# Kernel optimization log

Hardware: AMD Instinct MI355X
Metric: run time of the kernel (lower is better)

Reference implementation:

```python
import jax, jax.numpy as jnp
import numpy as np

N_NODES = 10000
N_EDGES = 70000
IN_DIM = 10
HEADS = 6
LIN_OUT = 254
GAT_DIMS = [(256, 508), (512, 250), (256, 120), (128, 20)]  # (in_dim, out_dim) per DeformGAT
NEG_SLOPE = 0.2


def setup_inputs() -> dict:
    key = jax.random.key(0)
    ks = jax.random.split(key, 8)
    inp = {}
    inp["data"] = jax.random.normal(ks[0], (N_NODES, IN_DIM), dtype=jnp.float32)
    inp["edge_idx"] = jax.random.randint(ks[1], (2, N_EDGES), 0, N_NODES)
    inp["bd_mask"] = jax.random.randint(ks[2], (N_NODES,), 0, 2) > 0
    inp["poly_mesh"] = 0
    inp["W_lin"] = jax.random.normal(ks[3], (IN_DIM, LIN_OUT), dtype=jnp.float32) * 0.05
    inp["b_lin"] = jnp.zeros((LIN_OUT,), dtype=jnp.float32)
    for i, (din, dout) in enumerate(GAT_DIMS):
        k1, k2, k3 = jax.random.split(ks[4 + i], 3)
        inp[f"W{i+1}"] = jax.random.normal(k1, (din, HEADS * dout), dtype=jnp.float32) * 0.05
        inp[f"asrc{i+1}"] = jax.random.normal(k2, (HEADS, dout), dtype=jnp.float32) * 0.05
        inp[f"adst{i+1}"] = jax.random.normal(k3, (HEADS, dout), dtype=jnp.float32) * 0.05
    return inp


def deform_gat(coord, feat, src, dst, bd_mask, W, a_src, a_dst, n):
    """One DeformGAT layer: GAT attention over edge list; features aggregated
    (head-averaged, SELU); coords moved to attention-weighted neighbor centroid,
    boundary nodes pinned."""
    H, C = a_src.shape
    x = (feat @ W).reshape(-1, H, C)                       # [N,H,C]
    a_s = jnp.einsum('nhc,hc->nh', x, a_src)               # [N,H]
    a_d = jnp.einsum('nhc,hc->nh', x, a_dst)               # [N,H]
    e = jax.nn.leaky_relu(a_s[src] + a_d[dst], NEG_SLOPE)  # [E,H]
    # segment softmax over incoming edges of each dst node
    m = jax.ops.segment_max(e, dst, num_segments=n)
    m = jnp.where(jnp.isfinite(m), m, 0.0)
    ex = jnp.exp(e - m[dst])
    denom = jax.ops.segment_sum(ex, dst, num_segments=n)
    alpha = ex / jnp.where(denom[dst] > 0, denom[dst], 1.0)        # [E,H]
    agg = jax.ops.segment_sum(alpha[:, :, None] * x[src], dst, num_segments=n)  # [N,H,C]
    out_feat = jax.nn.selu(agg.mean(axis=1))                       # [N,C]
    am = alpha.mean(axis=1)                                        # [E]
    new_coord = jax.ops.segment_sum(am[:, None] * coord[src], dst, num_segments=n)  # [N,2]
    out_coord = jnp.where(bd_mask[:, None], coord, new_coord)
    return out_coord, out_feat


def reference(data, edge_idx, bd_mask, poly_mesh, W_lin, b_lin,
              W1, asrc1, adst1, W2, asrc2, adst2,
              W3, asrc3, adst3, W4, asrc4, adst4):
    n = data.shape[0]
    coords = data[:, 0:2]
    src, dst = edge_idx[0], edge_idx[1]
    h = jax.nn.selu(data @ W_lin + b_lin)                  # [N,254]
    t1 = jnp.concatenate([coords, h], axis=1)              # [N,256]
    c1, f1 = deform_gat(coords, t1, src, dst, bd_mask, W1, asrc1, adst1, n)
    t2 = jnp.concatenate([c1, coords, f1], axis=1)         # [N,512]
    c2, f2 = deform_gat(c1, t2, src, dst, bd_mask, W2, asrc2, adst2, n)
    t3 = jnp.concatenate([c2, c1, coords, f2], axis=1)     # [N,256]
    c3, f3 = deform_gat(c2, t3, src, dst, bd_mask, W3, asrc3, adst3, n)
    t4 = jnp.concatenate([c3, c2, c1, coords, f3], axis=1) # [N,128]
    c4, f4 = deform_gat(c3, t4, src, dst, bd_mask, W4, asrc4, adst4, n)
    return c4
```

## Files before the change

kernel.cpp:

```cpp
#include <hip/hip_runtime.h>
#include <hip/hip_bf16.h>

#define N_NODES 10000
#define N_EDGES 70000
#define HEADS 6
#define MPAD 10112
#define SELU_SCALE 1.0507009873554805f
#define SELU_ALPHA  1.6732632423543772f
#define NEG_SLOPE 0.2f

typedef __attribute__((ext_vector_type(8))) __bf16 bf16x8;
typedef __attribute__((ext_vector_type(4))) float f32x4;

__device__ __forceinline__ float selu_f(float x) {
    return x > 0.f ? SELU_SCALE * x : SELU_SCALE * SELU_ALPHA * (__expf(x) - 1.f);
}
__device__ __forceinline__ unsigned short f2bf(float f) {
    __hip_bfloat16 h = __float2bfloat16(f);
    return __builtin_bit_cast(unsigned short, h);
}
__device__ __forceinline__ float bf2f(unsigned short u) {
    unsigned int x = ((unsigned int)u) << 16;
    return __builtin_bit_cast(float, x);
}

__global__ void count_edges_k(const int* __restrict__ dstv, int* __restrict__ counts) {
    int e = blockIdx.x * blockDim.x + threadIdx.x;
    if (e < N_EDGES) atomicAdd(&counts[dstv[e]], 1);
}

__global__ __launch_bounds__(1024) void scan_k(const int* __restrict__ counts, int* __restrict__ offs) {
    __shared__ int part[1024];
    int tid = threadIdx.x;
    const int per = (N_NODES + 1023) / 1024;
    int start = tid * per;
    int s = 0;
    for (int i = 0; i < per; ++i) { int idx = start + i; if (idx < N_NODES) s += counts[idx]; }
    part[tid] = s;
    __syncthreads();
    for (int off = 1; off < 1024; off <<= 1) {
        int v = (tid >= off) ? part[tid - off] : 0;
        __syncthreads();
        part[tid] += v;
        __syncthreads();
    }
    int run = part[tid] - s;
    for (int i = 0; i < per; ++i) {
        int idx = start + i;
        if (idx < N_NODES) { offs[idx] = run; run += counts[idx]; }
    }
    if (tid == 0) offs[N_NODES] = part[1023];
}

__global__ void fill_csr_k(const int* __restrict__ srcv, const int* __restrict__ dstv,
                           const int* __restrict__ offs,
                           int* __restrict__ cursor, int* __restrict__ srcs) {
    int e = blockIdx.x * blockDim.x + threadIdx.x;
    if (e < N_EDGES) {
        int d = dstv[e];
        int pos = atomicAdd(&cursor[d], 1);
        srcs[offs[d] + pos] = srcv[e];
    }
}

__global__ __launch_bounds__(256) void prep_proj_k(
    const float* __restrict__ data, const float* __restrict__ W, const float* __restrict__ b,
    float* __restrict__ coords0, unsigned short* __restrict__ t1,
    const float* __restrict__ wsf, const float* __restrict__ wdf,
    float* __restrict__ a_s, float* __restrict__ a_d) {
    const int wid = threadIdx.x >> 6, lane = threadIdx.x & 63;
    const int n = blockIdx.x * 4 + wid;
    if (n >= N_NODES) return;
    const int c0 = lane * 4;
    const float* dr = data + (size_t)n * 10;

    float vals[4];
#pragma unroll
    for (int q = 0; q < 4; ++q) {
        int c = c0 + q;
        if (c < 2) {
            vals[q] = dr[c];
        } else {
            int cc = c - 2;
            float acc = b[cc];
#pragma unroll
            for (int k = 0; k < 10; ++k) acc += dr[k] * W[k * 254 + cc];
            vals[q] = selu_f(acc);
        }
    }
    uint2 pk;
    pk.x = (unsigned int)f2bf(vals[0]) | ((unsigned int)f2bf(vals[1]) << 16);
    pk.y = (unsigned int)f2bf(vals[2]) | ((unsigned int)f2bf(vals[3]) << 16);
    *(uint2*)(t1 + (size_t)n * 256 + c0) = pk;
    if (lane == 0) {
        coords0[2 * n] = vals[0];
        coords0[2 * n + 1] = vals[1];
    }

    float s[HEADS] = {}, d[HEADS] = {};
#pragma unroll
    for (int q = 0; q < 4; ++q) {
        float v = bf2f(f2bf(vals[q]));
        const float* ws = wsf + (size_t)(c0 + q) * HEADS;
        const float* wd = wdf + (size_t)(c0 + q) * HEADS;
#pragma unroll
        for (int h = 0; h < HEADS; ++h) {
            s[h] += v * ws[h];
            d[h] += v * wd[h];
        }
    }
#pragma unroll
    for (int off = 32; off > 0; off >>= 1) {
#pragma unroll
        for (int h = 0; h < HEADS; ++h) {
            s[h] += __shfl_xor(s[h], off);
            d[h] += __shfl_xor(d[h], off);
        }
    }
    if (lane == 0) {
#pragma unroll
        for (int h = 0; h < HEADS; ++h) {
            a_s[n * HEADS + h] = s[h];
            a_d[n * HEADS + h] = d[h];
        }
    }
}

__global__ __launch_bounds__(256) void weights_prep_k(
    const float* __restrict__ W0, const float* __restrict__ s0v, const float* __restrict__ d0v,
    const float* __restrict__ W1, const float* __restrict__ s1v, const float* __restrict__ d1v,
    const float* __restrict__ W2, const float* __restrict__ s2v, const float* __restrict__ d2v,
    const float* __restrict__ W3, const float* __restrict__ s3v, const float* __restrict__ d3v,
    float* __restrict__ wsf0, float* __restrict__ wdf0,
    float* __restrict__ wsf1, float* __restrict__ wdf1,
    float* __restrict__ wsf2, float* __restrict__ wdf2,
    float* __restrict__ wsf3, float* __restrict__ wdf3,
    unsigned short* __restrict__ Vt0, unsigned short* __restrict__ Vt1,
    unsigned short* __restrict__ Vt2) {
    __shared__ float tile[64][65];
    const int bidg = blockIdx.x;
    if (bidg < 1728) {
        const int wid = threadIdx.x >> 6, lane = threadIdx.x & 63;
        int bid = bidg * 4 + wid;
        const float* W; const float* sv; const float* dv; float* ws; float* wd;
        int K, C, pair;
        if (bid < 1536)      { W = W0; sv = s0v; dv = d0v; ws = wsf0; wd = wdf0; K = 256; C = 508; pair = bid; }
        else if (bid < 4608) { W = W1; sv = s1v; dv = d1v; ws = wsf1; wd = wdf1; K = 512; C = 250; pair = bid - 1536; }
        else if (bid < 6144) { W = W2; sv = s2v; dv = d2v; ws = wsf2; wd = wdf2; K = 256; C = 120; pair = bid - 4608; }
        else                 { W = W3; sv = s3v; dv = d3v; ws = wsf3; wd = wdf3; K = 128; C = 20;  pair = bid - 6144; }
        int k = pair / HEADS, h = pair % HEADS;
        const float* wr = W + (size_t)k * (HEADS * C) + h * C;
        const float* sr = sv + h * C;
        const float* dr = dv + h * C;
        float s = 0.f, d = 0.f;
        for (int c = lane; c < C; c += 64) {
            float w = wr[c];
            s += w * sr[c];
            d += w * dr[c];
        }
#pragma unroll
        for (int off = 32; off > 0; off >>= 1) {
            s += __shfl_xor(s, off);
            d += __shfl_xor(d, off);
        }
        if (lane == 0) { ws[pair] = s; wd[pair] = d; }
    } else {
        int bid = bidg - 1728;
        const float* W; unsigned short* Vt; int K, C, K6, bid2, ktiles;
        if (bid < 192)      { W = W0; Vt = Vt0; K = 256; C = 508; K6 = 1536; bid2 = bid;       ktiles = 24; }
        else if (bid < 384) { W = W1; Vt = Vt1; K = 512; C = 250; K6 = 3072; bid2 = bid - 192; ktiles = 48; }
        else                { W = W2; Vt = Vt2; K = 256; C = 120; K6 = 1536; bid2 = bid - 384; ktiles = 24; }
        int kb = bid2 % ktiles, cb = bid2 / ktiles;
        const int tx = threadIdx.x & 63;
        const int ty = threadIdx.x >> 6;
        const int k0 = kb * 64;
        const int c0 = cb * 64;
        for (int i = ty; i < 64; i += 4) {
            int kk = k0 + i;
            int h = kk / K, k = kk - h * K;
            int c = c0 + tx;
            tile[i][tx] = (c < C) ? W[(size_t)k * (HEADS * C) + h * C + c] : 0.f;
        }
        __syncthreads();
        for (int i = ty; i < 64; i += 4) {
            int c = c0 + i;
            Vt[(size_t)c * K6 + k0 + tx] = f2bf(tile[tx][i]);
        }
    }
}

__global__ __launch_bounds__(256) void gemm_split_k(
    const unsigned short* __restrict__ A,
    const unsigned short* __restrict__ Bt,
    unsigned short* __restrict__ part,
    int Kpitch, int klen, int Npad) {
    __shared__ unsigned short lds[2][16384];
    const int tid = threadIdx.x;
    const int lane = tid & 63, wid = tid >> 6;
    const int wm = wid >> 1, wn = wid & 1;
    const int m0 = blockIdx.y * 128;
    const int n0 = blockIdx.x * 128;
    const int kz = blockIdx.z;
    const int kbeg = kz * klen;
    const int nt = klen >> 6;

    f32x4 acc[4][4] = {};

    const unsigned short* gsrc[8];
    unsigned ldsoff[8];
#pragma unroll
    for (int i = 0; i < 8; ++i) {
        const int half = i >> 2;
        const int slot = (i & 3) * 256 + tid;
        const int r = slot >> 3;
        const int c16 = slot & 7;
        const int ksl = c16 ^ (r & 7);
        gsrc[i] = (half ? (Bt + (size_t)(n0 + r) * Kpitch) : (A + (size_t)(m0 + r) * Kpitch)) + ksl * 8;
        ldsoff[i] = (unsigned)(half * 8192 + ((i & 3) * 256 + wid * 64) * 8);
    }

    auto stage = [&](int kt, int buf) {
#pragma unroll
        for (int i = 0; i < 8; ++i) {
            __builtin_amdgcn_global_load_lds(
                (const __attribute__((address_space(1))) unsigned int*)(gsrc[i] + kt),
                (__attribute__((address_space(3))) unsigned int*)(&lds[buf][ldsoff[i]]),
                16, 0, 0);
        }
    };

    stage(kbeg, 0);
    for (int t = 0; t < nt; ++t) {
        const int cur = t & 1;
        if (t + 1 < nt) {
            stage(kbeg + (t + 1) * 64, cur ^ 1);
            asm volatile("s_waitcnt vmcnt(8)" ::: "memory");
        } else {
            asm volatile("s_waitcnt vmcnt(0)" ::: "memory");
        }
        __builtin_amdgcn_sched_barrier(0);
        __builtin_amdgcn_s_barrier();
        const char* base = (const char*)(&lds[cur][0]);
#pragma unroll
        for (int kc = 0; kc < 2; ++kc) {
            const int xo = (((kc * 4 + (lane >> 4)) ^ (lane & 7)) << 4);
            bf16x8 aop[4], bop[4];
#pragma unroll
            for (int f = 0; f < 4; ++f) {
                const int rA = wm * 64 + f * 16 + (lane & 15);
                bop[f] = *(const bf16x8*)(base + rA * 128 + xo);
                const int rB = wn * 64 + f * 16 + (lane & 15);
                aop[f] = *(const bf16x8*)(base + 16384 + rB * 128 + xo);
            }
#pragma unroll
            for (int fm = 0; fm < 4; ++fm)
#pragma unroll
                for (int fn = 0; fn < 4; ++fn)
                    acc[fm][fn] = __builtin_amdgcn_mfma_f32_16x16x32_bf16(
                        aop[fn], bop[fm], acc[fm][fn], 0, 0, 0);
        }
        __builtin_amdgcn_s_barrier();
    }

    unsigned short* pbase = part + (size_t)kz * MPAD * Npad;
    const int mrow = m0 + wm * 64 + (lane & 15);
    const int ncol = n0 + wn * 64 + ((lane >> 4) * 4);
#pragma unroll
    for (int fm = 0; fm < 4; ++fm) {
#pragma unroll
        for (int fn = 0; fn < 4; ++fn) {
            f32x4 v = acc[fm][fn];
            unsigned int u0 = (unsigned int)f2bf(v.x) | ((unsigned int)f2bf(v.y) << 16);
            unsigned int u1 = (unsigned int)f2bf(v.z) | ((unsigned int)f2bf(v.w) << 16);
            uint2 pk = make_uint2(u0, u1);
            *(uint2*)&pbase[(size_t)(mrow + fm * 16) * Npad + ncol + fn * 16] = pk;
        }
    }
}

template<int KN>
__global__ __launch_bounds__(256) void reduceproj_k(
    const unsigned short* __restrict__ part, int KS, int Npad, int off,
    unsigned short* __restrict__ tnext,
    const float* __restrict__ wsf, const float* __restrict__ wdf,
    float* __restrict__ a_s, float* __restrict__ a_d) {
    const int wid = threadIdx.x >> 6, lane = threadIdx.x & 63;
    const int n = blockIdx.x * 4 + wid;
    if (n >= N_NODES) return;
    constexpr int KPL = KN / 64;
    const int c0 = lane * KPL;
    unsigned short* row = tnext + (size_t)n * KN;

    float vals[KPL];
#pragma unroll
    for (int q = 0; q < KPL; q += 2) {
        int c = c0 + q;
        if (c < off) {
            unsigned int u = *(const unsigned int*)(row + c);
            vals[q] = bf2f((unsigned short)(u & 0xffff));
            vals[q + 1] = bf2f((unsigned short)(u >> 16));
        } else {
            int cp = c - off;
            float s0 = 0.f, s1 = 0.f;
            for (int kz = 0; kz < KS; ++kz) {
                unsigned int u = *(const unsigned int*)(part + (size_t)kz * MPAD * Npad
                                                       + (size_t)n * Npad + cp);
                s0 += bf2f((unsigned short)(u & 0xffff));
                s1 += bf2f((unsigned short)(u >> 16));
            }
            float o0 = selu_f(s0 * (1.f / 6.f));
            float o1 = selu_f(s1 * (1.f / 6.f));
            vals[q] = o0; vals[q + 1] = o1;
            *(unsigned int*)(row + c) =
                (unsigned int)f2bf(o0) | ((unsigned int)f2bf(o1) << 16);
        }
    }

    float s[HEADS] = {}, d[HEADS] = {};
#pragma unroll
    for (int q = 0; q < KPL; ++q) {
        int c = c0 + q;
        float v = vals[q];
        const float* ws = wsf + (size_t)c * HEADS;
        const float* wd = wdf + (size_t)c * HEADS;
#pragma unroll
        for (int h = 0; h < HEADS; ++h) {
            s[h] += v * ws[h];
            d[h] += v * wd[h];
        }
    }
#pragma unroll
    for (int off2 = 32; off2 > 0; off2 >>= 1) {
#pragma unroll
        for (int h = 0; h < HEADS; ++h) {
            s[h] += __shfl_xor(s[h], off2);
            d[h] += __shfl_xor(d[h], off2);
        }
    }
    if (lane == 0) {
#pragma unroll
        for (int h = 0; h < HEADS; ++h) {
            a_s[n * HEADS + h] = s[h];
            a_d[n * HEADS + h] = d[h];
        }
    }
}

template<int KT>
__global__ __launch_bounds__(256) void attn_agg_move_k(
    const float* __restrict__ a_s, const float* __restrict__ a_d,
    const int* __restrict__ srcs, const int* __restrict__ offs,
    const unsigned short* __restrict__ t_in, unsigned short* __restrict__ thagg,
    const float* __restrict__ cprev, const int* __restrict__ bd,
    float* __restrict__ cout, unsigned short* __restrict__ tnext, int ld,
    const float* __restrict__ xA, int offA,
    const float* __restrict__ xB, int offB) {
    const int wid = threadIdx.x >> 6, lane = threadIdx.x & 63;
    const int n = blockIdx.x * 4 + wid;
    if (n >= N_NODES) return;
    const int r0 = offs[n], r1 = offs[n + 1];
    const int deg = r1 - r0;

    float ad[HEADS];
#pragma unroll
    for (int h = 0; h < HEADS; ++h) ad[h] = a_d[n * HEADS + h];

    constexpr int KPL = (KT > 0) ? (KT / 64) : 1;
    float acc[HEADS][KPL] = {};
    float cx = 0.f, cy = 0.f;

    if (deg <= 64) {
        const bool ok = lane < deg;
        const int mysrc = ok ? srcs[r0 + lane] : 0;
        float lv[HEADS], mm[HEADS], ss[HEADS], myal[HEADS];
#pragma unroll
        for (int h = 0; h < HEADS; ++h) {
            float v = -1e30f;
            if (ok) {
                v = a_s[mysrc * HEADS + h] + ad[h];
                v = v > 0.f ? v : NEG_SLOPE * v;
            }
            lv[h] = v;
            mm[h] = v;
        }
#pragma unroll
        for (int off = 32; off > 0; off >>= 1)
#pragma unroll
            for (int h = 0; h < HEADS; ++h) mm[h] = fmaxf(mm[h], __shfl_xor(mm[h], off));
#pragma unroll
        for (int h = 0; h < HEADS; ++h) {
            myal[h] = ok ? __expf(lv[h] - mm[h]) : 0.f;
            ss[h] = myal[h];
        }
#pragma unroll
        for (int off = 32; off > 0; off >>= 1)
#pragma unroll
            for (int h = 0; h < HEADS; ++h) ss[h] += __shfl_xor(ss[h], off);
        float am = 0.f;
#pragma unroll
        for (int h = 0; h < HEADS; ++h) {
            float rdh = ss[h] > 0.f ? 1.f / ss[h] : 0.f;
            myal[h] *= rdh;
            am += myal[h];
        }
        if (ok) {
            am *= (1.f / 6.f);
            cx = am * cprev[2 * mysrc];
            cy = am * cprev[2 * mysrc + 1];
        }
        if constexpr (KT > 0) {
            for (int j = 0; j < deg; ++j) {
                int src = __shfl(mysrc, j);
                float al[HEADS];
#pragma unroll
                for (int h = 0; h < HEADS; ++h) al[h] = __shfl(myal[h], j);
                if constexpr (KT == 512) {
                    uint4 u = *(const uint4*)(t_in + (size_t)src * 512 + lane * 8);
                    float tv[8];
                    tv[0] = bf2f((unsigned short)(u.x & 0xffff)); tv[1] = bf2f((unsigned short)(u.x >> 16));
                    tv[2] = bf2f((unsigned short)(u.y & 0xffff)); tv[3] = bf2f((unsigned short)(u.y >> 16));
                    tv[4] = bf2f((unsigned short)(u.z & 0xffff)); tv[5] = bf2f((unsigned short)(u.z >> 16));
                    tv[6] = bf2f((unsigned short)(u.w & 0xffff)); tv[7] = bf2f((unsigned short)(u.w >> 16));
#pragma unroll
                    for (int h = 0; h < HEADS; ++h)
#pragma unroll
                        for (int q = 0; q < 8; ++q) acc[h][q] += al[h] * tv[q];
                } else {
                    uint2 u = *(const uint2*)(t_in + (size_t)src * 256 + lane * 4);
                    float tv[4];
                    tv[0] = bf2f((unsigned short)(u.x & 0xffff)); tv[1] = bf2f((unsigned short)(u.x >> 16));
                    tv[2] = bf2f((unsigned short)(u.y & 0xffff)); tv[3] = bf2f((unsigned short)(u.y >> 16));
#pragma unroll
                    for (int h = 0; h < HEADS; ++h)
#pragma unroll
                        for (int q = 0; q < 4; ++q) acc[h][q] += al[h] * tv[q];
                }
            }
        }
    } else {
        float mm[HEADS], ss[HEADS];
#pragma unroll
        for (int h = 0; h < HEADS; ++h) { mm[h] = -1e30f; ss[h] = 0.f; }
        for (int base = r0; base < r1; base += 64) {
            int i = base + lane;
            if (i < r1) {
                int src = srcs[i];
#pragma unroll
                for (int h = 0; h < HEADS; ++h) {
                    float v = a_s[src * HEADS + h] + ad[h];
                    v = v > 0.f ? v : NEG_SLOPE * v;
                    float nm = fmaxf(mm[h], v);
                    ss[h] = ss[h] * __expf(mm[h] - nm) + __expf(v - nm);
                    mm[h] = nm;
                }
            }
        }
#pragma unroll
        for (int off = 32; off > 0; off >>= 1) {
#pragma unroll
            for (int h = 0; h < HEADS; ++h) {
                float mo = __shfl_xor(mm[h], off);
                float so = __shfl_xor(ss[h], off);
                float nm = fmaxf(mm[h], mo);
                ss[h] = ss[h] * __expf(mm[h] - nm) + so * __expf(mo - nm);
                mm[h] = nm;
            }
        }
        float rd[HEADS];
#pragma unroll
        for (int h = 0; h < HEADS; ++h) rd[h] = ss[h] > 0.f ? 1.f / ss[h] : 0.f;

        for (int base = r0; base < r1; base += 64) {
            int i = base + lane;
            bool ok = i < r1;
            int mysrc = ok ? srcs[i] : 0;
            float myal[HEADS];
#pragma unroll
            for (int h = 0; h < HEADS; ++h) myal[h] = 0.f;
            if (ok) {
                float am = 0.f;
#pragma unroll
                for (int h = 0; h < HEADS; ++h) {
                    float v = a_s[mysrc * HEADS + h] + ad[h];
                    v = v > 0.f ? v : NEG_SLOPE * v;
                    float a = __expf(v - mm[h]) * rd[h];
                    myal[h] = a;
                    am += a;
                }
                am *= (1.f / 6.f);
                cx += am * cprev[2 * mysrc];
                cy += am * cprev[2 * mysrc + 1];
            }
            if constexpr (KT > 0) {
                int cnt = min(64, r1 - base);
                for (int j = 0; j < cnt; ++j) {
                    int src = __shfl(mysrc, j);
                    float al[HEADS];
#pragma unroll
                    for (int h = 0; h < HEADS; ++h) al[h] = __shfl(myal[h], j);
                    if constexpr (KT == 512) {
                        uint4 u = *(const uint4*)(t_in + (size_t)src * 512 + lane * 8);
                        float tv[8];
                        tv[0] = bf2f((unsigned short)(u.x & 0xffff)); tv[1] = bf2f((unsigned short)(u.x >> 16));
                        tv[2] = bf2f((unsigned short)(u.y & 0xffff)); tv[3] = bf2f((unsigned short)(u.y >> 16));
                        tv[4] = bf2f((unsigned short)(u.z & 0xffff)); tv[5] = bf2f((unsigned short)(u.z >> 16));
                        tv[6] = bf2f((unsigned short)(u.w & 0xffff)); tv[7] = bf2f((unsigned short)(u.w >> 16));
#pragma unroll
                        for (int h = 0; h < HEADS; ++h)
#pragma unroll
                            for (int q = 0; q < 8; ++q) acc[h][q] += al[h] * tv[q];
                    } else {
                        uint2 u = *(const uint2*)(t_in + (size_t)src * 256 + lane * 4);
                        float tv[4];
                        tv[0] = bf2f((unsigned short)(u.x & 0xffff)); tv[1] = bf2f((unsigned short)(u.x >> 16));
                        tv[2] = bf2f((unsigned short)(u.y & 0xffff)); tv[3] = bf2f((unsigned short)(u.y >> 16));
#pragma unroll
                        for (int h = 0; h < HEADS; ++h)
#pragma unroll
                            for (int q = 0; q < 4; ++q) acc[h][q] += al[h] * tv[q];
                    }
                }
            }
        }
    }

    if constexpr (KT == 512) {
#pragma unroll
        for (int h = 0; h < HEADS; ++h) {
            uint4 pk;
            pk.x = (unsigned int)f2bf(acc[h][0]) | ((unsigned int)f2bf(acc[h][1]) << 16);
            pk.y = (unsigned int)f2bf(acc[h][2]) | ((unsigned int)f2bf(acc[h][3]) << 16);
            pk.z = (unsigned int)f2bf(acc[h][4]) | ((unsigned int)f2bf(acc[h][5]) << 16);
            pk.w = (unsigned int)f2bf(acc[h][6]) | ((unsigned int)f2bf(acc[h][7]) << 16);
            *(uint4*)(thagg + (size_t)n * 3072 + h * 512 + lane * 8) = pk;
        }
    } else if constexpr (KT == 256) {
#pragma unroll
        for (int h = 0; h < HEADS; ++h) {
            uint2 pk;
            pk.x = (unsigned int)f2bf(acc[h][0]) | ((unsigned int)f2bf(acc[h][1]) << 16);
            pk.y = (unsigned int)f2bf(acc[h][2]) | ((unsigned int)f2bf(acc[h][3]) << 16);
            *(uint2*)(thagg + (size_t)n * 1536 + h * 256 + lane * 4) = pk;
        }
    }
#pragma unroll
    for (int off = 32; off > 0; off >>= 1) {
        cx += __shfl_xor(cx, off);
        cy += __shfl_xor(cy, off);
    }
    if (lane == 0) {
        float px = cprev[2 * n], py = cprev[2 * n + 1];
        float ocx, ocy;
        if (bd[n] != 0) { ocx = px; ocy = py; }
        else { ocx = cx; ocy = cy; }
        cout[2 * n] = ocx; cout[2 * n + 1] = ocy;
        if (tnext) {
            unsigned short* row = tnext + (size_t)n * ld;
            row[0] = f2bf(ocx); row[1] = f2bf(ocy);
            row[2] = f2bf(px);  row[3] = f2bf(py);
            if (xA) { row[offA] = f2bf(xA[2 * n]); row[offA + 1] = f2bf(xA[2 * n + 1]); }
            if (xB) { row[offB] = f2bf(xB[2 * n]); row[offB + 1] = f2bf(xB[2 * n + 1]); }
        }
    }
}

static inline int cdiv(int a, int b) { return (a + b - 1) / b; }

extern "C" void kernel_launch(void* const* d_in, const int* in_sizes, int n_in,
                              void* d_out, int out_size, void* d_ws, size_t ws_size,
                              hipStream_t stream) {
    const float* data = (const float*)d_in[0];
    const int* eidx = (const int*)d_in[1];
    const int* bd = (const int*)d_in[2];
    const float* W_lin = (const float*)d_in[4];
    const float* b_lin = (const float*)d_in[5];
    const float* Wl[4]  = {(const float*)d_in[6],  (const float*)d_in[9],
                           (const float*)d_in[12], (const float*)d_in[15]};
    const float* Asrc[4] = {(const float*)d_in[7],  (const float*)d_in[10],
                            (const float*)d_in[13], (const float*)d_in[16]};
    const float* Adst[4] = {(const float*)d_in[8],  (const float*)d_in[11],
                            (const float*)d_in[14], (const float*)d_in[17]};
    const int Kd[4] = {256, 512, 256, 128};
    const int Cpadd[4] = {512, 256, 128, 0};
    const int KSd[4] = {2, 4, 4, 0};

    const int* srcv = eidx;
    const int* dstv = eidx + N_EDGES;

    char* p = (char*)d_ws;
    auto alloc = [&](size_t bytes) -> void* {
        void* r = (void*)p;
        p += (bytes + 255) & ~(size_t)255;
        return r;
    };
    unsigned short* tb1 = (unsigned short*)alloc((size_t)MPAD * 256 * 2);
    unsigned short* tb2 = (unsigned short*)alloc((size_t)MPAD * 512 * 2);
    unsigned short* tb3 = (unsigned short*)alloc((size_t)MPAD * 256 * 2);
    unsigned short* tb4 = (unsigned short*)alloc((size_t)MPAD * 128 * 2);
    unsigned short* thagg = (unsigned short*)alloc((size_t)MPAD * 3072 * 2);
    unsigned short* VtL[3];
    VtL[0] = (unsigned short*)alloc((size_t)512 * 1536 * 2);
    VtL[1] = (unsigned short*)alloc((size_t)256 * 3072 * 2);
    VtL[2] = (unsigned short*)alloc((size_t)128 * 1536 * 2);
    unsigned short* partb = (unsigned short*)alloc((size_t)8 * MPAD * 256 * 2);
    float* coords0 = (float*)alloc((size_t)N_NODES * 2 * 4);
    float* c1 = (float*)alloc((size_t)N_NODES * 2 * 4);
    float* c2 = (float*)alloc((size_t)N_NODES * 2 * 4);
    float* c3 = (float*)alloc((size_t)N_NODES * 2 * 4);
    float* a_s = (float*)alloc((size_t)N_NODES * HEADS * 4);
    float* a_d = (float*)alloc((size_t)N_NODES * HEADS * 4);
    float* wsfL[4]; float* wdfL[4];
    wsfL[0] = (float*)alloc(1536 * 4); wdfL[0] = (float*)alloc(1536 * 4);
    wsfL[1] = (float*)alloc(3072 * 4); wdfL[1] = (float*)alloc(3072 * 4);
    wsfL[2] = (float*)alloc(1536 * 4); wdfL[2] = (float*)alloc(1536 * 4);
    wsfL[3] = (float*)alloc(768 * 4);  wdfL[3] = (float*)alloc(768 * 4);
    int* counts = (int*)alloc((size_t)N_NODES * 4);
    int* cursor = (int*)alloc((size_t)N_NODES * 4);
    int* offs = (int*)alloc((size_t)(N_NODES + 1) * 4);
    int* srcs = (int*)alloc((size_t)N_EDGES * 4);

    hipMemsetAsync(counts, 0, (size_t)((char*)offs - (char*)counts), stream);
    count_edges_k<<<cdiv(N_EDGES, 256), 256, 0, stream>>>(dstv, counts);
    scan_k<<<1, 1024, 0, stream>>>(counts, offs);
    fill_csr_k<<<cdiv(N_EDGES, 256), 256, 0, stream>>>(srcv, dstv, offs, cursor, srcs);

    weights_prep_k<<<2160, 256, 0, stream>>>(
        Wl[0], Asrc[0], Adst[0], Wl[1], Asrc[1], Adst[1],
        Wl[2], Asrc[2], Adst[2], Wl[3], Asrc[3], Adst[3],
        wsfL[0], wdfL[0], wsfL[1], wdfL[1], wsfL[2], wdfL[2], wsfL[3], wdfL[3],
        VtL[0], VtL[1], VtL[2]);
    prep_proj_k<<<cdiv(N_NODES, 4), 256, 0, stream>>>(
        data, W_lin, b_lin, coords0, tb1, wsfL[0], wdfL[0], a_s, a_d);

    unsigned short* tin[4]   = {tb1, tb2, tb3, tb4};
    unsigned short* tnext[4] = {tb2, tb3, tb4, nullptr};
    int ldn[4]  = {512, 256, 128, 0};
    int foff[4] = {4, 6, 8, 0};
    float* cprev[4] = {coords0, c1, c2, c3};
    float* cout[4]  = {c1, c2, c3, (float*)d_out};
    const float* xAv[4] = {nullptr, coords0, c1, nullptr};
    int offAv[4] = {0, 4, 4, 0};
    const float* xBv[4] = {nullptr, nullptr, coords0, nullptr};
    int offBv[4] = {0, 0, 6, 0};

    for (int l = 0; l < 4; ++l) {
        int K = Kd[l], Cpad = Cpadd[l], KS = KSd[l];
        int K6 = K * HEADS;

        if (l == 3) {
            attn_agg_move_k<0><<<cdiv(N_NODES, 4), 256, 0, stream>>>(
                a_s, a_d, srcs, offs, tin[l], nullptr,
                cprev[l], bd, cout[l], tnext[l], ldn[l],
                xAv[l], offAv[l], xBv[l], offBv[l]);
        } else if (K == 512) {
            attn_agg_move_k<512><<<cdiv(N_NODES, 4), 256, 0, stream>>>(
                a_s, a_d, srcs, offs, tin[l], thagg,
                cprev[l], bd, cout[l], tnext[l], ldn[l],
                xAv[l], offAv[l], xBv[l], offBv[l]);
        } else {
            attn_agg_move_k<256><<<cdiv(N_NODES, 4), 256, 0, stream>>>(
                a_s, a_d, srcs, offs, tin[l], thagg,
                cprev[l], bd, cout[l], tnext[l], ldn[l],
                xAv[l], offAv[l], xBv[l], offBv[l]);
        }

        if (l < 3) {
            int klen = K6 / KS;
            gemm_split_k<<<dim3(Cpad / 128, MPAD / 128, KS), 256, 0, stream>>>(
                thagg, VtL[l], partb, K6, klen, Cpad);
            if (ldn[l] == 512) {
                reduceproj_k<512><<<cdiv(N_NODES, 4), 256, 0, stream>>>(
                    partb, KS, Cpad, foff[l], tnext[l], wsfL[l + 1], wdfL[l + 1], a_s, a_d);
            } else if (ldn[l] == 256) {
                reduceproj_k<256><<<cdiv(N_NODES, 4), 256, 0, stream>>>(
                    partb, KS, Cpad, foff[l], tnext[l], wsfL[l + 1], wdfL[l + 1], a_s, a_d);
            } else {
                reduceproj_k<128><<<cdiv(N_NODES, 4), 256, 0, stream>>>(
                    partb, KS, Cpad, foff[l], tnext[l], wsfL[l + 1], wdfL[l + 1], a_s, a_d);
            }
        }
    }
}
```

Baseline: 299.3 us.

## Replace split-K GEMM with direct GEMM and fused SELU epilogue for first two layers

```diff
diff --git a/kernel.cpp b/kernel.cpp
--- a/kernel.cpp
+++ b/kernel.cpp
@@ -189,6 +189,112 @@
     }
 }
 
+struct GemmCtx {
+    const unsigned short* gsrc[8];
+    unsigned ldsoff[8];
+};
+
+__global__ __launch_bounds__(256) void gemm_direct_k(
+    const unsigned short* __restrict__ A,
+    const unsigned short* __restrict__ Bt,
+    unsigned short* __restrict__ outT,
+    int Kpitch, int ld, int off, int Cfeat) {
+    __shared__ unsigned short lds[2][16384];
+    const int tid = threadIdx.x;
+    const int lane = tid & 63, wid = tid >> 6;
+    const int wm = wid >> 1, wn = wid & 1;
+    const int m0 = blockIdx.y * 128;
+    const int n0 = blockIdx.x * 128;
+    const int nt = Kpitch >> 6;
+
+    f32x4 acc[4][4] = {};
+
+    const unsigned short* gsrc[8];
+    unsigned ldsoff[8];
+#pragma unroll
+    for (int i = 0; i < 8; ++i) {
+        const int half = i >> 2;
+        const int slot = (i & 3) * 256 + tid;
+        const int r = slot >> 3;
+        const int c16 = slot & 7;
+        const int ksl = c16 ^ (r & 7);
+        gsrc[i] = (half ? (Bt + (size_t)(n0 + r) * Kpitch) : (A + (size_t)(m0 + r) * Kpitch)) + ksl * 8;
+        ldsoff[i] = (unsigned)(half * 8192 + ((i & 3) * 256 + wid * 64) * 8);
+    }
+
+    auto stage = [&](int kt, int buf) {
+#pragma unroll
+        for (int i = 0; i < 8; ++i) {
+            __builtin_amdgcn_global_load_lds(
+                (const __attribute__((address_space(1))) unsigned int*)(gsrc[i] + kt),
+                (__attribute__((address_space(3))) unsigned int*)(&lds[buf][ldsoff[i]]),
+                16, 0, 0);
+        }
+    };
+
+    stage(0, 0);
+    for (int t = 0; t < nt; ++t) {
+        const int cur = t & 1;
+        if (t + 1 < nt) {
+            stage((t + 1) * 64, cur ^ 1);
+            asm volatile("s_waitcnt vmcnt(8)" ::: "memory");
+        } else {
+            asm volatile("s_waitcnt vmcnt(0)" ::: "memory");
+        }
+        __builtin_amdgcn_sched_barrier(0);
+        __builtin_amdgcn_s_barrier();
+        const char* base = (const char*)(&lds[cur][0]);
+#pragma unroll
+        for (int kc = 0; kc < 2; ++kc) {
+            const int xo = (((kc * 4 + (lane >> 4)) ^ (lane & 7)) << 4);
+            bf16x8 aop[4], bop[4];
+#pragma unroll
+            for (int f = 0; f < 4; ++f) {
+                const int rA = wm * 64 + f * 16 + (lane & 15);
+                bop[f] = *(const bf16x8*)(base + rA * 128 + xo);
+                const int rB = wn * 64 + f * 16 + (lane & 15);
+                aop[f] = *(const bf16x8*)(base + 16384 + rB * 128 + xo);
+            }
+#pragma unroll
+            for (int fm = 0; fm < 4; ++fm)
+#pragma unroll
+                for (int fn = 0; fn < 4; ++fn)
+                    acc[fm][fn] = __builtin_amdgcn_mfma_f32_16x16x32_bf16(
+                        aop[fn], bop[fm], acc[fm][fn], 0, 0, 0);
+        }
+        __builtin_amdgcn_s_barrier();
+    }
+
+    const int mrow = m0 + wm * 64 + (lane & 15);
+    const int ncol = n0 + wn * 64 + ((lane >> 4) * 4);
+#pragma unroll
+    for (int fm = 0; fm < 4; ++fm) {
+        int r = mrow + fm * 16;
+        unsigned short* row = outT + (size_t)r * ld + off;
+#pragma unroll
+        for (int fn = 0; fn < 4; ++fn) {
+            int cb = ncol + fn * 16;
+            f32x4 v = acc[fm][fn];
+            float o[4];
+            o[0] = selu_f(v.x * (1.f / 6.f));
+            o[1] = selu_f(v.y * (1.f / 6.f));
+            o[2] = selu_f(v.z * (1.f / 6.f));
+            o[3] = selu_f(v.w * (1.f / 6.f));
+#pragma unroll
+            for (int e = 0; e < 4; e += 2) {
+                int c = cb + e;
+                if (c + 1 < Cfeat) {
+                    *(unsigned int*)(row + c) =
+                        (unsigned int)f2bf(o[e]) | ((unsigned int)f2bf(o[e + 1]) << 16);
+                } else {
+                    if (c < Cfeat) row[c] = f2bf(o[e]);
+                    if (c + 1 < Cfeat) row[c + 1] = f2bf(o[e + 1]);
+                }
+            }
+        }
+    }
+}
+
 __global__ __launch_bounds__(256) void gemm_split_k(
     const unsigned short* __restrict__ A,
     const unsigned short* __restrict__ Bt,
@@ -274,6 +380,62 @@
             unsigned int u1 = (unsigned int)f2bf(v.z) | ((unsigned int)f2bf(v.w) << 16);
             uint2 pk = make_uint2(u0, u1);
             *(uint2*)&pbase[(size_t)(mrow + fm * 16) * Npad + ncol + fn * 16] = pk;
+        }
+    }
+}
+
+__global__ __launch_bounds__(256) void proj2_k(const unsigned short* __restrict__ t,
+                                               const float* __restrict__ wsf,
+                                               const float* __restrict__ wdf,
+                                               float* __restrict__ a_s,
+                                               float* __restrict__ a_d, int K) {
+    const int wv = threadIdx.x >> 6;
+    const int lane = threadIdx.x & 63;
+    const int n = blockIdx.x * 4 + wv;
+    if (n >= N_NODES) return;
+    const unsigned short* tr = t + (size_t)n * K;
+    const int kpl = K >> 6;
+    const int k0 = lane * kpl;
+
+    unsigned int buf[4] = {0u, 0u, 0u, 0u};
+    if (kpl == 8) {
+        uint4 u = *(const uint4*)(tr + k0);
+        buf[0] = u.x; buf[1] = u.y; buf[2] = u.z; buf[3] = u.w;
+    } else if (kpl == 4) {
+        uint2 u = *(const uint2*)(tr + k0);
+        buf[0] = u.x; buf[1] = u.y;
+    } else {
+        buf[0] = *(const unsigned int*)(tr + k0);
+    }
+
+    float s[HEADS] = {}, d[HEADS] = {};
+#pragma unroll
+    for (int j = 0; j < 8; ++j) {
+        if (j >= kpl) break;
+        unsigned int w = buf[j >> 1];
+        unsigned short u = (j & 1) ? (unsigned short)(w >> 16) : (unsigned short)(w & 0xffff);
+        float v = bf2f(u);
+        const float* ws = wsf + (size_t)(k0 + j) * HEADS;
+        const float* wd = wdf + (size_t)(k0 + j) * HEADS;
+#pragma unroll
+        for (int h = 0; h < HEADS; ++h) {
+            s[h] += v * ws[h];
+            d[h] += v * wd[h];
+        }
+    }
+#pragma unroll
+    for (int off = 32; off > 0; off >>= 1) {
+#pragma unroll
+        for (int h = 0; h < HEADS; ++h) {
+            s[h] += __shfl_xor(s[h], off);
+            d[h] += __shfl_xor(d[h], off);
+        }
+    }
+    if (lane == 0) {
+#pragma unroll
+        for (int h = 0; h < HEADS; ++h) {
+            a_s[n * HEADS + h] = s[h];
+            a_d[n * HEADS + h] = d[h];
         }
     }
 }
@@ -581,8 +743,8 @@
     const float* Adst[4] = {(const float*)d_in[8],  (const float*)d_in[11],
                             (const float*)d_in[14], (const float*)d_in[17]};
     const int Kd[4] = {256, 512, 256, 128};
+    const int Cd[4] = {508, 250, 120, 20};
     const int Cpadd[4] = {512, 256, 128, 0};
-    const int KSd[4] = {2, 4, 4, 0};
 
     const int* srcv = eidx;
     const int* dstv = eidx + N_EDGES;
@@ -602,7 +764,7 @@
     VtL[0] = (unsigned short*)alloc((size_t)512 * 1536 * 2);
     VtL[1] = (unsigned short*)alloc((size_t)256 * 3072 * 2);
     VtL[2] = (unsigned short*)alloc((size_t)128 * 1536 * 2);
-    unsigned short* partb = (unsigned short*)alloc((size_t)8 * MPAD * 256 * 2);
+    unsigned short* partb = (unsigned short*)alloc((size_t)4 * MPAD * 128 * 2);
     float* coords0 = (float*)alloc((size_t)N_NODES * 2 * 4);
     float* c1 = (float*)alloc((size_t)N_NODES * 2 * 4);
     float* c2 = (float*)alloc((size_t)N_NODES * 2 * 4);
@@ -644,7 +806,7 @@
     int offBv[4] = {0, 0, 6, 0};
 
     for (int l = 0; l < 4; ++l) {
-        int K = Kd[l], Cpad = Cpadd[l], KS = KSd[l];
+        int K = Kd[l], C = Cd[l], Cpad = Cpadd[l];
         int K6 = K * HEADS;
 
         if (l == 3) {
@@ -664,20 +826,18 @@
                 xAv[l], offAv[l], xBv[l], offBv[l]);
         }
 
-        if (l < 3) {
+        if (l < 2) {
+            gemm_direct_k<<<dim3(Cpad / 128, MPAD / 128), 256, 0, stream>>>(
+                thagg, VtL[l], tnext[l], K6, ldn[l], foff[l], C);
+            proj2_k<<<cdiv(N_NODES, 4), 256, 0, stream>>>(
+                tnext[l], wsfL[l + 1], wdfL[l + 1], a_s, a_d, ldn[l]);
+        } else if (l == 2) {
+            const int KS = 4;
             int klen = K6 / KS;
             gemm_split_k<<<dim3(Cpad / 128, MPAD / 128, KS), 256, 0, stream>>>(
                 thagg, VtL[l], partb, K6, klen, Cpad);
-            if (ldn[l] == 512) {
-                reduceproj_k<512><<<cdiv(N_NODES, 4), 256, 0, stream>>>(
-                    partb, KS, Cpad, foff[l], tnext[l], wsfL[l + 1], wdfL[l + 1], a_s, a_d);
-            } else if (ldn[l] == 256) {
-                reduceproj_k<256><<<cdiv(N_NODES, 4), 256, 0, stream>>>(
-                    partb, KS, Cpad, foff[l], tnext[l], wsfL[l + 1], wdfL[l + 1], a_s, a_d);
-            } else {
-                reduceproj_k<128><<<cdiv(N_NODES, 4), 256, 0, stream>>>(
-                    partb, KS, Cpad, foff[l], tnext[l], wsfL[l + 1], wdfL[l + 1], a_s, a_d);
-            }
-        }
-    }
-}
+            reduceproj_k<128><<<cdiv(N_NODES, 4), 256, 0, stream>>>(
+                partb, KS, Cpad, foff[l], tnext[l], wsfL[l + 1], wdfL[l + 1], a_s, a_d);
+        }
+    }
+}
```

After: 301.1 us. Within noise of the previous version (+0.6%).
